# Kernel optimization log

Measured on AMD Instinct MI355X. Metric: run time of the kernel, lower is better.

Reference implementation:

```python
import jax, jax.numpy as jnp
import numpy as np
from jax import lax

B, T, V, E, H = 64, 20, 32000, 256, 512
EPS = 1e-5


def _conv_bn_relu(x, w, b, g, beta, m, v):
    # x: (B,C,H,W), w: (O,I,3,3), stride 2, pad 1; BN in eval mode with running stats
    y = lax.conv_general_dilated(x, w, (2, 2), ((1, 1), (1, 1)),
                                 dimension_numbers=('NCHW', 'OIHW', 'NCHW'))
    y = y + b[None, :, None, None]
    inv = g / jnp.sqrt(v + EPS)
    y = y * inv[None, :, None, None] + (beta - m * inv)[None, :, None, None]
    return jax.nn.relu(y)


def setup_inputs() -> dict:
    key = jax.random.key(0)
    ks = iter(jax.random.split(key, 40))
    s = 0.05
    d = {}
    d['images'] = jax.random.normal(next(ks), (B, 3, 64, 64), jnp.float32)
    d['captions'] = jax.random.randint(next(ks), (B, T), 0, V)
    chans = [3, 64, 128, 256, 512]
    for i in range(4):
        ci, co = chans[i], chans[i + 1]
        d[f'conv{i+1}_w'] = jax.random.normal(next(ks), (co, ci, 3, 3), jnp.float32) * s
        d[f'conv{i+1}_b'] = jnp.zeros((co,), jnp.float32)
        d[f'bn{i+1}_g'] = jnp.ones((co,), jnp.float32)
        d[f'bn{i+1}_b'] = jnp.zeros((co,), jnp.float32)
        d[f'bn{i+1}_m'] = jnp.zeros((co,), jnp.float32)
        d[f'bn{i+1}_v'] = jnp.ones((co,), jnp.float32)
    d['proj_w'] = jax.random.normal(next(ks), (E, 512), jnp.float32) * s
    d['proj_b'] = jnp.zeros((E,), jnp.float32)
    d['emb'] = jax.random.normal(next(ks), (V, E), jnp.float32) * s
    d['att_wv'] = jax.random.normal(next(ks), (H, E), jnp.float32) * s
    d['att_bv'] = jnp.zeros((H,), jnp.float32)
    d['att_wt'] = jax.random.normal(next(ks), (H, H), jnp.float32) * s
    d['att_bt'] = jnp.zeros((H,), jnp.float32)
    d['att_wa'] = jax.random.normal(next(ks), (1, H), jnp.float32) * s
    d['att_ba'] = jnp.zeros((1,), jnp.float32)
    d['w_ih'] = jax.random.normal(next(ks), (4 * H, 2 * E), jnp.float32) * s
    d['w_hh'] = jax.random.normal(next(ks), (4 * H, H), jnp.float32) * s
    d['b_ih'] = jnp.zeros((4 * H,), jnp.float32)
    d['b_hh'] = jnp.zeros((4 * H,), jnp.float32)
    d['out_w'] = jax.random.normal(next(ks), (V, H), jnp.float32) * s
    d['out_b'] = jnp.zeros((V,), jnp.float32)
    return d


def reference(images, captions,
              conv1_w, conv1_b, bn1_g, bn1_b, bn1_m, bn1_v,
              conv2_w, conv2_b, bn2_g, bn2_b, bn2_m, bn2_v,
              conv3_w, conv3_b, bn3_g, bn3_b, bn3_m, bn3_v,
              conv4_w, conv4_b, bn4_g, bn4_b, bn4_m, bn4_v,
              proj_w, proj_b, emb,
              att_wv, att_bv, att_wt, att_bt, att_wa, att_ba,
              w_ih, w_hh, b_ih, b_hh, out_w, out_b):
    # --- image encoder ---
    x = _conv_bn_relu(images, conv1_w, conv1_b, bn1_g, bn1_b, bn1_m, bn1_v)
    x = _conv_bn_relu(x, conv2_w, conv2_b, bn2_g, bn2_b, bn2_m, bn2_v)
    x = _conv_bn_relu(x, conv3_w, conv3_b, bn3_g, bn3_b, bn3_m, bn3_v)
    x = _conv_bn_relu(x, conv4_w, conv4_b, bn4_g, bn4_b, bn4_m, bn4_v)  # (B,512,4,4)
    b, c, h_, w_ = x.shape
    visual = x.reshape(b, c, h_ * w_).transpose(0, 2, 1)  # (B,R=16,512)
    visual = visual @ proj_w.T + proj_b                    # (B,R,E)

    v_proj = visual @ att_wv.T + att_bv                    # (B,R,H) - precompute

    emb_seq = emb[captions].transpose(1, 0, 2)             # (T,B,E)

    def step(carry, word_embed):
        h, cst = carry
        # attention over regions conditioned on previous h
        t = h @ att_wt.T + att_bt                          # (B,H)
        comb = jnp.tanh(v_proj + t[:, None, :])            # (B,R,H)
        scores = jnp.einsum('brh,h->br', comb, att_wa[0]) + att_ba[0]
        attw = jax.nn.softmax(scores, axis=1)              # (B,R)
        attended = jnp.einsum('br,bre->be', attw, visual)  # (B,E)
        xin = jnp.concatenate([word_embed, attended], axis=1)  # (B,2E)
        gates = xin @ w_ih.T + b_ih + h @ w_hh.T + b_hh    # (B,4H)
        i, f, g, o = jnp.split(gates, 4, axis=1)           # torch gate order i,f,g,o
        cst = jax.nn.sigmoid(f) * cst + jax.nn.sigmoid(i) * jnp.tanh(g)
        h = jax.nn.sigmoid(o) * jnp.tanh(cst)
        logits = h @ out_w.T + out_b                       # (B,V)
        return (h, cst), logits

    h0 = jnp.zeros((b, H), visual.dtype)
    c0 = jnp.zeros((b, H), visual.dtype)
    _, logits = lax.scan(step, (h0, c0), emb_seq)          # (T,B,V)
    return logits.transpose(1, 0, 2)                       # (B,T,V)
```

## Files before the change

kernel.cpp:

```cpp
#include <hip/hip_runtime.h>
#include <hip/hip_bf16.h>
#include <cstdint>
#include <cstddef>

typedef __attribute__((ext_vector_type(8))) short short8;
typedef __attribute__((ext_vector_type(4))) float floatx4;

__device__ inline float bf2f(unsigned short u) {
  union { unsigned int i; float f; } v; v.i = ((unsigned int)u) << 16; return v.f;
}
__device__ inline unsigned short f2bf(float f) {
  union { float f; unsigned int i; } v; v.f = f;
  unsigned int u = v.i;
  return (unsigned short)((u + 0x7FFFu + ((u >> 16) & 1u)) >> 16);
}
__device__ inline short8 ld8(const unsigned short* p) {
  return *reinterpret_cast<const short8*>(p);
}
__device__ inline float sigmoidf_(float x) { return 1.0f / (1.0f + expf(-x)); }

#define AT_LD(p)    __hip_atomic_load((p), __ATOMIC_RELAXED, __HIP_MEMORY_SCOPE_AGENT)
#define AT_ST(p, v) __hip_atomic_store((p), (v), __ATOMIC_RELAXED, __HIP_MEMORY_SCOPE_AGENT)
#define WAITCNT0()  asm volatile("s_waitcnt vmcnt(0) lgkmcnt(0)" ::: "memory")

static const size_t OFF_WIH   = 0;
static const size_t OFF_WHH   = 2097152;
static const size_t OFF_VPROJ = 4194304;
static const size_t OFF_VISE  = 5242880;
static const size_t OFF_HS    = 5767168;
static const size_t OFF_XIN   = 7077888;
static const size_t OFF_H0    = 7143424;
static const size_t OFF_H1    = 7208960;
static const size_t OFF_CT    = 7274496;
static const size_t OFF_W1PAD = 7405568;
static const size_t OFF_CW2   = 7409664;
static const size_t OFF_CW3   = 7557120;
static const size_t OFF_CW4   = 8146944;
static const size_t OFF_PRJW  = 10506240;
static const size_t OFF_ATWV  = 10768384;
static const size_t OFF_ACT1  = 11030528;
static const size_t OFF_ACT3  = 11030528;
static const size_t OFF_ACT2  = 19419136;
static const size_t OFF_ACT4  = 19419136;
static const size_t OFF_VISA  = 20467712;
static const size_t OFF_COL   = 23613440;
static const size_t OFF_BAR   = 28332032;
static const size_t OFF_ATWT  = 28348416;
static const size_t OFF_BIG   = 28872704;
static const size_t NEED_BIG  = OFF_BIG + 32768000;

__device__ inline void grid_bar(unsigned int* bar, unsigned int gen) {
  WAITCNT0();
  __syncthreads();
  if (threadIdx.x == 0)
    AT_ST(bar + (size_t)blockIdx.x * 32, gen);
  if (blockIdx.x == 0 && threadIdx.x < 64) {
    while (AT_LD(bar + (size_t)threadIdx.x * 32) < gen) __builtin_amdgcn_s_sleep(1);
    if (threadIdx.x == 0) AT_ST(bar + 2048, gen);
  }
  if (threadIdx.x == 0) {
    while (AT_LD(bar + 2048) < gen) __builtin_amdgcn_s_sleep(1);
  }
  __syncthreads();
  asm volatile("" ::: "memory");
}

__global__ void cvt_k(const float* __restrict__ s, unsigned short* __restrict__ d, int n4)
{
  int i = blockIdx.x * 256 + threadIdx.x;
  if (i < n4) {
    float4 v = reinterpret_cast<const float4*>(s)[i];
    ushort4 o;
    o.x = f2bf(v.x); o.y = f2bf(v.y); o.z = f2bf(v.z); o.w = f2bf(v.w);
    reinterpret_cast<ushort4*>(d)[i] = o;
  }
}

struct CvtArgs {
  const float* s[8];
  unsigned short* d[8];
  int cum[9];
};
__global__ void cvtall_k(CvtArgs a)
{
  int i = blockIdx.x * 256 + threadIdx.x;
  if (i >= a.cum[8]) return;
  int seg = 0;
  while (seg < 7 && i >= a.cum[seg + 1]) ++seg;
  int j = i - a.cum[seg];
  float4 v = reinterpret_cast<const float4*>(a.s[seg])[j];
  ushort4 o;
  o.x = f2bf(v.x); o.y = f2bf(v.y); o.z = f2bf(v.z); o.w = f2bf(v.w);
  reinterpret_cast<ushort4*>(a.d[seg])[j] = o;
}

__global__ void init_k(const float* __restrict__ conv1_w, unsigned short* __restrict__ w1pad,
                       unsigned short* __restrict__ h0, float* __restrict__ cT,
                       unsigned int* __restrict__ bar)
{
  int i = blockIdx.x * 256 + threadIdx.x;
  if (i < 64 * 32) {
    int co = i >> 5, k = i & 31;
    w1pad[i] = (k < 27) ? f2bf(conv1_w[co * 27 + k]) : (unsigned short)0;
  }
  if (i < 64 * 512) h0[i] = 0;
  if (i < 512 * 64) cT[i] = 0.0f;
  if (i < 4096) bar[i] = 0u;
}

__global__ void im2col1_k(const float* __restrict__ in, unsigned short* __restrict__ col)
{
  int o = blockIdx.x * 256 + threadIdx.x;
  int n = o >> 5, k = o & 31;
  unsigned short v = 0;
  if (k < 27) {
    int b = n >> 10, y = (n >> 5) & 31, x = n & 31;
    int ci = k / 9, r9 = k - ci * 9, ky = r9 / 3, kx = r9 - ky * 3;
    int iy = 2 * y - 1 + ky, ix = 2 * x - 1 + kx;
    if (iy >= 0 && iy < 64 && ix >= 0 && ix < 64)
      v = f2bf(in[(((size_t)b * 3 + ci) << 12) + (iy << 6) + ix]);
  }
  col[o] = v;
}

__global__ void im2col_k(const unsigned short* __restrict__ in, unsigned short* __restrict__ col,
                         int Cin, int Hin, int Win, int Kreal, int Kpad, int lgHW, int lgW,
                         int n0)
{
  const int ng = n0 + blockIdx.x;
  const int b = ng >> lgHW;
  const int yx = ng & ((1 << lgHW) - 1);
  const int y = yx >> lgW;
  const int x = yx & ((1 << lgW) - 1);
  const int iy0 = 2 * y - 1;
  const int ix0 = 2 * x - 1;
  for (int k = threadIdx.x; k < Kpad; k += blockDim.x) {
    unsigned short v = 0;
    if (k < Kreal) {
      int ci = k / 9;
      int r9 = k - ci * 9;
      int ky = r9 / 3;
      int kx = r9 - ky * 3;
      int iy = iy0 + ky, ix = ix0 + kx;
      if (iy >= 0 && iy < Hin && ix >= 0 && ix < Win) {
        size_t idx = (((size_t)b * Cin + ci) * Hin + iy) * Win + ix;
        v = in[idx];
      }
    }
    col[(size_t)blockIdx.x * Kpad + k] = v;
  }
}

__global__ void visa_k(const unsigned short* __restrict__ act4, unsigned short* __restrict__ visA)
{
  int o = blockIdx.x * 256 + threadIdx.x;
  int c = o & 511, br = o >> 9;
  int b = br >> 4, r = br & 15;
  visA[o] = act4[(((size_t)b * 512 + c) << 4) + r];
}

template<int EPI>
__global__ __launch_bounds__(256)
void gemm_k(const unsigned short* __restrict__ A, const unsigned short* __restrict__ B,
            int K, int N, void* __restrict__ outp,
            const float* __restrict__ cb, const float* __restrict__ bg,
            const float* __restrict__ bb, const float* __restrict__ bm,
            const float* __restrict__ bv, int Cout, int lgHW,
            const float* __restrict__ biasN, int n_base, int ldOut)
{
  const int w   = threadIdx.x >> 6;
  const int l   = threadIdx.x & 63;
  const int l15 = l & 15;
  const int q   = l >> 4;
  const int m0  = blockIdx.y * 64;
  const int n0  = blockIdx.x * 256 + w * 64;
  const unsigned short* Ap = A + (size_t)(m0 + l15) * K + q * 8;
  const unsigned short* Bp = B + (size_t)(n0 + l15) * K + q * 8;

  floatx4 acc[4][4];
  #pragma unroll
  for (int i = 0; i < 4; i++)
    #pragma unroll
    for (int j = 0; j < 4; j++)
      acc[i][j] = (floatx4){0.f, 0.f, 0.f, 0.f};

  for (int kc = 0; kc < K; kc += 32) {
    short8 a0 = ld8(Ap + kc);
    short8 a1 = ld8(Ap + (size_t)16 * K + kc);
    short8 a2 = ld8(Ap + (size_t)32 * K + kc);
    short8 a3 = ld8(Ap + (size_t)48 * K + kc);
    #pragma unroll
    for (int nf = 0; nf < 4; nf++) {
      short8 bf = ld8(Bp + (size_t)(nf * 16) * K + kc);
      acc[0][nf] = __builtin_amdgcn_mfma_f32_16x16x32_bf16(a0, bf, acc[0][nf], 0, 0, 0);
      acc[1][nf] = __builtin_amdgcn_mfma_f32_16x16x32_bf16(a1, bf, acc[1][nf], 0, 0, 0);
      acc[2][nf] = __builtin_amdgcn_mfma_f32_16x16x32_bf16(a2, bf, acc[2][nf], 0, 0, 0);
      acc[3][nf] = __builtin_amdgcn_mfma_f32_16x16x32_bf16(a3, bf, acc[3][nf], 0, 0, 0);
    }
  }
  #pragma unroll
  for (int mf = 0; mf < 4; mf++) {
    #pragma unroll
    for (int r = 0; r < 4; r++) {
      int m = m0 + mf * 16 + q * 4 + r;
      float scale = 1.0f, shift = 0.0f;
      if (EPI == 0) {
        float inv = bg[m] / sqrtf(bv[m] + 1e-5f);
        scale = inv;
        shift = (cb[m] - bm[m]) * inv + bb[m];
      }
      #pragma unroll
      for (int nf = 0; nf < 4; nf++) {
        int n = n0 + nf * 16 + l15;
        float c = acc[mf][nf][r];
        if (EPI == 0) {
          c = fmaxf(c * scale + shift, 0.0f);
          int ng = n_base + n;
          int bi = ng >> lgHW;
          int yx = ng & ((1 << lgHW) - 1);
          ((unsigned short*)outp)[(((size_t)bi * Cout + m) << lgHW) + yx] = f2bf(c);
        } else if (EPI == 1) {
          ((unsigned short*)outp)[(size_t)m * N + n] = f2bf(c + biasN[n]);
        } else {
          ((float*)outp)[(size_t)m * ldOut + n_base + n] = c + biasN[n_base + n];
        }
      }
    }
  }
}

__global__ __launch_bounds__(256)
void rec_k(const unsigned short* __restrict__ w_ih, const unsigned short* __restrict__ w_hh,
           const float* __restrict__ b_ih, const float* __restrict__ b_hh,
           const unsigned short* __restrict__ vproj, const unsigned short* __restrict__ visE,
           const unsigned short* __restrict__ atwt, const float* __restrict__ att_bt,
           const float* __restrict__ att_wa, const float* __restrict__ att_ba,
           const int* __restrict__ captions, const float* __restrict__ emb,
           unsigned int* xin_u, unsigned int* h0_u, unsigned int* h1_u,
           float* __restrict__ cT, unsigned short* __restrict__ hs,
           unsigned int* __restrict__ bar)
{
  __shared__ __align__(16) float sH[512];
  __shared__ float sT[512];
  __shared__ float sA[256];
  __shared__ float sSc[16];
  __shared__ float sAw[16];
  __shared__ __align__(16) unsigned short sB[16384];
  __shared__ float sG[4][16][64];

  const int tid = threadIdx.x;
  const int bid = blockIdx.x;
  const int w   = tid >> 6;
  const int l   = tid & 63;
  const int l15 = l & 15;
  const int q   = l >> 4;
  const int u0  = bid * 16;
  const int arow = w * 512 + u0 + l15;

  for (int t = 0; t < 20; ++t) {
    unsigned int* hin_u  = (t & 1) ? h1_u : h0_u;
    unsigned int* hout_u = (t & 1) ? h0_u : h1_u;

    {
      const int b = bid;
      unsigned int hv = AT_LD(hin_u + b * 256 + tid);
      sH[2 * tid]     = bf2f((unsigned short)(hv & 0xffffu));
      sH[2 * tid + 1] = bf2f((unsigned short)(hv >> 16));
      __syncthreads();

      {
        const unsigned short* w0 = atwt + (size_t)tid * 512;
        const unsigned short* w1 = w0 + (size_t)256 * 512;
        float a0 = 0.f, a1 = 0.f;
        #pragma unroll 2
        for (int k = 0; k < 512; k += 8) {
          short8 x0 = ld8(w0 + k);
          short8 x1 = ld8(w1 + k);
          #pragma unroll
          for (int j = 0; j < 8; ++j) {
            float hk = sH[k + j];
            a0 += bf2f((unsigned short)x0[j]) * hk;
            a1 += bf2f((unsigned short)x1[j]) * hk;
          }
        }
        sT[tid]       = a0 + att_bt[tid];
        sT[tid + 256] = a1 + att_bt[tid + 256];
      }
      __syncthreads();

      {
        int r = tid >> 4, l16 = tid & 15;
        const unsigned short* vp = vproj + ((size_t)b * 16 + r) * 512;
        float s = 0.0f;
        int k0 = l16 * 32;
        for (int k = k0; k < k0 + 32; k++)
          s += tanhf(bf2f(vp[k]) + sT[k]) * att_wa[k];
        for (int d = 8; d >= 1; d >>= 1) s += __shfl_down(s, d, 16);
        if (l16 == 0) sSc[r] = s + att_ba[0];
      }
      __syncthreads();

      if (tid < 16) {
        float s = sSc[tid];
        float m = s;
        for (int d = 8; d >= 1; d >>= 1) m = fmaxf(m, __shfl_xor(m, d, 16));
        float e = expf(s - m);
        float sum = e;
        for (int d = 8; d >= 1; d >>= 1) sum += __shfl_xor(sum, d, 16);
        sAw[tid] = e / sum;
      }
      __syncthreads();

      {
        float a = 0.0f;
        #pragma unroll
        for (int r = 0; r < 16; r++)
          a += sAw[r] * bf2f(visE[((size_t)b * 16 + r) * 256 + tid]);
        sA[tid] = a;
      }
      __syncthreads();

      if (tid < 128) {
        int cap = captions[b * 20 + t];
        float2 ev = *reinterpret_cast<const float2*>(emb + (size_t)cap * 256 + 2 * tid);
        AT_ST(xin_u + b * 256 + tid,
              (unsigned int)f2bf(ev.x) | ((unsigned int)f2bf(ev.y) << 16));
      } else {
        int j2 = 2 * (tid - 128);
        AT_ST(xin_u + b * 256 + tid,
              (unsigned int)f2bf(sA[j2]) | ((unsigned int)f2bf(sA[j2 + 1]) << 16));
      }
    }
    grid_bar(bar, 2 * t + 1);

    if (bid < 32) {
      floatx4 acc[4];
      #pragma unroll
      for (int nt = 0; nt < 4; nt++) acc[nt] = (floatx4){0.f, 0.f, 0.f, 0.f};

      #pragma unroll
      for (int src = 0; src < 2; ++src) {
        unsigned int* Bu = src ? hin_u : xin_u;
        const unsigned short* Arow = (src ? w_hh : w_ih) + (size_t)arow * 512;
        #pragma unroll
        for (int half = 0; half < 2; ++half) {
          __syncthreads();
          for (int i = tid; i < 8192; i += 256) {
            int row = i >> 7, cu = i & 127;
            unsigned int v = AT_LD(Bu + row * 256 + half * 128 + cu);
            reinterpret_cast<unsigned int*>(sB)[(row * 128 + cu) ^ ((row & 7) << 2)] = v;
          }
          __syncthreads();
          const unsigned short* Ap = Arow + half * 256 + q * 8;
          #pragma unroll
          for (int kc = 0; kc < 256; kc += 32) {
            short8 a = ld8(Ap + kc);
            #pragma unroll
            for (int nt = 0; nt < 4; ++nt) {
              int row = l15 + nt * 16;
              short8 bf = *reinterpret_cast<const short8*>(
                  sB + (((size_t)row * 256 + q * 8 + kc) ^ ((row & 7) << 3)));
              acc[nt] = __builtin_amdgcn_mfma_f32_16x16x32_bf16(a, bf, acc[nt], 0, 0, 0);
            }
          }
        }
      }
      #pragma unroll
      for (int nt = 0; nt < 4; nt++)
        #pragma unroll
        for (int r = 0; r < 4; r++)
          sG[w][q * 4 + r][nt * 16 + l15] = acc[nt][r];
      __syncthreads();

      const int batch = tid & 63;
      const int g0 = tid >> 6;
      #pragma unroll
      for (int s = 0; s < 4; s += 2) {
        float hn2[2];
        #pragma unroll
        for (int d = 0; d < 2; ++d) {
          int um = g0 * 4 + s + d;
          int u = u0 + um;
          float ii = sG[0][um][batch] + b_ih[u]        + b_hh[u];
          float ff = sG[1][um][batch] + b_ih[512 + u]  + b_hh[512 + u];
          float gg = sG[2][um][batch] + b_ih[1024 + u] + b_hh[1024 + u];
          float oo = sG[3][um][batch] + b_ih[1536 + u] + b_hh[1536 + u];
          float co = cT[u * 64 + batch];
          float cn = sigmoidf_(ff) * co + sigmoidf_(ii) * tanhf(gg);
          hn2[d] = sigmoidf_(oo) * tanhf(cn);
          cT[u * 64 + batch] = cn;
        }
        int u = u0 + g0 * 4 + s;
        unsigned int hp = (unsigned int)f2bf(hn2[0]) | ((unsigned int)f2bf(hn2[1]) << 16);
        AT_ST(hout_u + batch * 256 + (u >> 1), hp);
        *reinterpret_cast<unsigned int*>(hs + ((size_t)batch * 20 + t) * 512 + u) = hp;
      }
    }
    grid_bar(bar, 2 * t + 2);
  }
}

extern "C" void kernel_launch(void* const* d_in, const int* in_sizes, int n_in,
                              void* d_out, int out_size, void* d_ws, size_t ws_size,
                              hipStream_t stream)
{
  const float* images   = (const float*)d_in[0];
  const int*   captions = (const int*)d_in[1];
  const float* cw[4] = {(const float*)d_in[2],  (const float*)d_in[8],
                        (const float*)d_in[14], (const float*)d_in[20]};
  const float* cbp[4] = {(const float*)d_in[3],  (const float*)d_in[9],
                         (const float*)d_in[15], (const float*)d_in[21]};
  const float* bgp[4] = {(const float*)d_in[4],  (const float*)d_in[10],
                         (const float*)d_in[16], (const float*)d_in[22]};
  const float* bbp[4] = {(const float*)d_in[5],  (const float*)d_in[11],
                         (const float*)d_in[17], (const float*)d_in[23]};
  const float* bmp[4] = {(const float*)d_in[6],  (const float*)d_in[12],
                         (const float*)d_in[18], (const float*)d_in[24]};
  const float* bvp[4] = {(const float*)d_in[7],  (const float*)d_in[13],
                         (const float*)d_in[19], (const float*)d_in[25]};
  const float* proj_w = (const float*)d_in[26];
  const float* proj_b = (const float*)d_in[27];
  const float* emb    = (const float*)d_in[28];
  const float* att_wv = (const float*)d_in[29];
  const float* att_bv = (const float*)d_in[30];
  const float* att_wt = (const float*)d_in[31];
  const float* att_bt = (const float*)d_in[32];
  const float* att_wa = (const float*)d_in[33];
  const float* att_ba = (const float*)d_in[34];
  const float* w_ih   = (const float*)d_in[35];
  const float* w_hh   = (const float*)d_in[36];
  const float* b_ih   = (const float*)d_in[37];
  const float* b_hh   = (const float*)d_in[38];
  const float* out_w  = (const float*)d_in[39];
  const float* out_b  = (const float*)d_in[40];

  char* W = (char*)d_ws;
  unsigned short* wih_b = (unsigned short*)(W + OFF_WIH);
  unsigned short* whh_b = (unsigned short*)(W + OFF_WHH);
  unsigned short* vproj = (unsigned short*)(W + OFF_VPROJ);
  unsigned short* visE  = (unsigned short*)(W + OFF_VISE);
  unsigned short* hs    = (unsigned short*)(W + OFF_HS);
  unsigned short* xin   = (unsigned short*)(W + OFF_XIN);
  unsigned short* h0    = (unsigned short*)(W + OFF_H0);
  unsigned short* h1    = (unsigned short*)(W + OFF_H1);
  float*          cT    = (float*)(W + OFF_CT);
  unsigned short* w1pad = (unsigned short*)(W + OFF_W1PAD);
  unsigned short* cw2_b = (unsigned short*)(W + OFF_CW2);
  unsigned short* cw3_b = (unsigned short*)(W + OFF_CW3);
  unsigned short* cw4_b = (unsigned short*)(W + OFF_CW4);
  unsigned short* prw_b = (unsigned short*)(W + OFF_PRJW);
  unsigned short* awv_b = (unsigned short*)(W + OFF_ATWV);
  unsigned short* atwt_b= (unsigned short*)(W + OFF_ATWT);
  unsigned short* act1  = (unsigned short*)(W + OFF_ACT1);
  unsigned short* act2  = (unsigned short*)(W + OFF_ACT2);
  unsigned short* act3  = (unsigned short*)(W + OFF_ACT3);
  unsigned short* act4  = (unsigned short*)(W + OFF_ACT4);
  unsigned short* visA  = (unsigned short*)(W + OFF_VISA);
  unsigned short* col   = (unsigned short*)(W + OFF_COL);
  unsigned int*   bar   = (unsigned int*)(W + OFF_BAR);
  const bool big = (ws_size >= NEED_BIG);
  unsigned short* colb  = big ? (unsigned short*)(W + OFF_BIG) : col;

  init_k<<<128, 256, 0, stream>>>(cw[0], w1pad, h0, cT, bar);

  {
    CvtArgs ca;
    ca.s[0] = w_ih;   ca.d[0] = wih_b;
    ca.s[1] = w_hh;   ca.d[1] = whh_b;
    ca.s[2] = cw[1];  ca.d[2] = cw2_b;
    ca.s[3] = cw[2];  ca.d[3] = cw3_b;
    ca.s[4] = cw[3];  ca.d[4] = cw4_b;
    ca.s[5] = proj_w; ca.d[5] = prw_b;
    ca.s[6] = att_wv; ca.d[6] = awv_b;
    ca.s[7] = att_wt; ca.d[7] = atwt_b;
    int c0 = 0;
    int cnt[8] = {262144, 262144, 18432, 73728, 294912, 32768, 32768, 65536};
    ca.cum[0] = 0;
    for (int i = 0; i < 8; i++) { c0 += cnt[i]; ca.cum[i + 1] = c0; }
    cvtall_k<<<(c0 + 255) / 256, 256, 0, stream>>>(ca);
  }

  im2col1_k<<<8192, 256, 0, stream>>>(images, col);
  gemm_k<0><<<dim3(256, 1), 256, 0, stream>>>(w1pad, col, 32, 65536, act1,
      cbp[0], bgp[0], bbp[0], bmp[0], bvp[0], 64, 10, nullptr, 0, 0);

  if (big) {
    im2col_k<<<16384, 256, 0, stream>>>(act1, colb, 64, 32, 32, 576, 576, 8, 4, 0);
    gemm_k<0><<<dim3(64, 2), 256, 0, stream>>>(cw2_b, colb, 576, 16384, act2,
        cbp[1], bgp[1], bbp[1], bmp[1], bvp[1], 128, 8, nullptr, 0, 0);
    im2col_k<<<4096, 256, 0, stream>>>(act2, colb, 128, 16, 16, 1152, 1152, 6, 3, 0);
    gemm_k<0><<<dim3(16, 4), 256, 0, stream>>>(cw3_b, colb, 1152, 4096, act3,
        cbp[2], bgp[2], bbp[2], bmp[2], bvp[2], 256, 6, nullptr, 0, 0);
  } else {
    for (int c = 0; c < 4; c++) {
      im2col_k<<<4096, 256, 0, stream>>>(act1, col, 64, 32, 32, 576, 576, 8, 4, c * 4096);
      gemm_k<0><<<dim3(16, 2), 256, 0, stream>>>(cw2_b, col, 576, 4096, act2,
          cbp[1], bgp[1], bbp[1], bmp[1], bvp[1], 128, 8, nullptr, c * 4096, 0);
    }
    for (int c = 0; c < 2; c++) {
      im2col_k<<<2048, 256, 0, stream>>>(act2, col, 128, 16, 16, 1152, 1152, 6, 3, c * 2048);
      gemm_k<0><<<dim3(8, 4), 256, 0, stream>>>(cw3_b, col, 1152, 2048, act3,
          cbp[2], bgp[2], bbp[2], bmp[2], bvp[2], 256, 6, nullptr, c * 2048, 0);
    }
  }
  im2col_k<<<1024, 256, 0, stream>>>(act3, col, 256, 8, 8, 2304, 2304, 4, 2, 0);
  gemm_k<0><<<dim3(4, 8), 256, 0, stream>>>(cw4_b, col, 2304, 1024, act4,
      cbp[3], bgp[3], bbp[3], bmp[3], bvp[3], 512, 4, nullptr, 0, 0);

  visa_k<<<2048, 256, 0, stream>>>(act4, visA);
  gemm_k<1><<<dim3(1, 16), 256, 0, stream>>>(visA, prw_b, 512, 256, visE,
      nullptr, nullptr, nullptr, nullptr, nullptr, 0, 0, proj_b, 0, 0);
  gemm_k<1><<<dim3(2, 16), 256, 0, stream>>>(visE, awv_b, 256, 512, vproj,
      nullptr, nullptr, nullptr, nullptr, nullptr, 0, 0, att_bv, 0, 0);

  rec_k<<<64, 256, 0, stream>>>(wih_b, whh_b, b_ih, b_hh, vproj, visE,
                                atwt_b, att_bt, att_wa, att_ba, captions, emb,
                                (unsigned int*)xin, (unsigned int*)h0, (unsigned int*)h1,
                                cT, hs, bar);

  if (big) {
    unsigned short* owb = (unsigned short*)(W + OFF_BIG);
    cvt_k<<<16000, 256, 0, stream>>>(out_w, owb, 32000 * 512 / 4);
    gemm_k<2><<<dim3(125, 20), 256, 0, stream>>>(hs, owb, 512, 32000,
        d_out, nullptr, nullptr, nullptr, nullptr, nullptr, 0, 0, out_b, 0, 32000);
  } else {
    for (int c = 0; c < 8; c++) {
      int rows = (c < 7) ? 4096 : 3328;
      const float* src = out_w + (size_t)c * 4096 * 512;
      cvt_k<<<rows / 2, 256, 0, stream>>>(src, col, rows * 512 / 4);
      gemm_k<2><<<dim3(rows / 256, 20), 256, 0, stream>>>(hs, col, 512, rows,
          d_out, nullptr, nullptr, nullptr, nullptr, nullptr, 0, 0, out_b, c * 4096, 32000);
    }
  }
}
```

Baseline: 1.884 ms.

## Replace grid barriers with per-block flags and overlap LSTM gate GEMM segments

The recurrent kernel drops its two full grid barriers per timestep and uses per-block step flags instead. Gate blocks wait only on the h flags, then run the word-embedding and W_hh parts of the gate product while attention is still running, and wait on the attention flags only before the attended-vector segment. The cell state moves from global memory into registers, bias sums are precomputed once, and tanh, exp and sigmoid use fast __expf approximations. This cuts serialization and global traffic in the latency-bound recurrence, at the cost of slightly lower accuracy and a more delicate memory-ordering protocol.

After: 1.687 ms. 10.5% less time.

```diff
diff --git a/kernel.cpp b/kernel.cpp
--- a/kernel.cpp
+++ b/kernel.cpp
@@ -17,11 +17,16 @@
 __device__ inline short8 ld8(const unsigned short* p) {
   return *reinterpret_cast<const short8*>(p);
 }
-__device__ inline float sigmoidf_(float x) { return 1.0f / (1.0f + expf(-x)); }
+__device__ inline float sigmoidf_(float x) { return 1.0f / (1.0f + __expf(-x)); }
+__device__ inline float tanh_fast(float x) {
+  float e = __expf(2.0f * x);
+  return 1.0f - 2.0f / (e + 1.0f);
+}
 
 #define AT_LD(p)    __hip_atomic_load((p), __ATOMIC_RELAXED, __HIP_MEMORY_SCOPE_AGENT)
 #define AT_ST(p, v) __hip_atomic_store((p), (v), __ATOMIC_RELAXED, __HIP_MEMORY_SCOPE_AGENT)
 #define WAITCNT0()  asm volatile("s_waitcnt vmcnt(0) lgkmcnt(0)" ::: "memory")
+#define CFENCE()    asm volatile("" ::: "memory")
 
 static const size_t OFF_WIH   = 0;
 static const size_t OFF_WHH   = 2097152;
@@ -49,22 +54,6 @@
 static const size_t OFF_BIG   = 28872704;
 static const size_t NEED_BIG  = OFF_BIG + 32768000;
 
-__device__ inline void grid_bar(unsigned int* bar, unsigned int gen) {
-  WAITCNT0();
-  __syncthreads();
-  if (threadIdx.x == 0)
-    AT_ST(bar + (size_t)blockIdx.x * 32, gen);
-  if (blockIdx.x == 0 && threadIdx.x < 64) {
-    while (AT_LD(bar + (size_t)threadIdx.x * 32) < gen) __builtin_amdgcn_s_sleep(1);
-    if (threadIdx.x == 0) AT_ST(bar + 2048, gen);
-  }
-  if (threadIdx.x == 0) {
-    while (AT_LD(bar + 2048) < gen) __builtin_amdgcn_s_sleep(1);
-  }
-  __syncthreads();
-  asm volatile("" ::: "memory");
-}
-
 __global__ void cvt_k(const float* __restrict__ s, unsigned short* __restrict__ d, int n4)
 {
   int i = blockIdx.x * 256 + threadIdx.x;
@@ -95,8 +84,7 @@
 }
 
 __global__ void init_k(const float* __restrict__ conv1_w, unsigned short* __restrict__ w1pad,
-                       unsigned short* __restrict__ h0, float* __restrict__ cT,
-                       unsigned int* __restrict__ bar)
+                       unsigned short* __restrict__ h0, unsigned int* __restrict__ bar)
 {
   int i = blockIdx.x * 256 + threadIdx.x;
   if (i < 64 * 32) {
@@ -104,7 +92,6 @@
     w1pad[i] = (k < 27) ? f2bf(conv1_w[co * 27 + k]) : (unsigned short)0;
   }
   if (i < 64 * 512) h0[i] = 0;
-  if (i < 512 * 64) cT[i] = 0.0f;
   if (i < 4096) bar[i] = 0u;
 }
 
@@ -237,16 +224,18 @@
            const float* __restrict__ att_wa, const float* __restrict__ att_ba,
            const int* __restrict__ captions, const float* __restrict__ emb,
            unsigned int* xin_u, unsigned int* h0_u, unsigned int* h1_u,
-           float* __restrict__ cT, unsigned short* __restrict__ hs,
-           unsigned int* __restrict__ bar)
+           unsigned short* __restrict__ hs, unsigned int* __restrict__ bar)
 {
   __shared__ __align__(16) float sH[512];
   __shared__ float sT[512];
   __shared__ float sA[256];
   __shared__ float sSc[16];
   __shared__ float sAw[16];
-  __shared__ __align__(16) unsigned short sB[16384];
+  __shared__ __align__(16) unsigned short sB[64 * 256];
   __shared__ float sG[4][16][64];
+
+  unsigned int* xf = bar;
+  unsigned int* hf = bar + 64;
 
   const int tid = threadIdx.x;
   const int bid = blockIdx.x;
@@ -256,10 +245,63 @@
   const int q   = l >> 4;
   const int u0  = bid * 16;
   const int arow = w * 512 + u0 + l15;
+  const unsigned short* wihRow = w_ih + (size_t)arow * 512;
+  const unsigned short* whhRow = w_hh + (size_t)arow * 512;
+
+  float creg[4];
+  float bsum[4][4];
+  if (bid < 32) {
+    const int batch = tid & 63;
+    const int g0 = tid >> 6;
+    (void)batch;
+    #pragma unroll
+    for (int s = 0; s < 4; ++s) {
+      creg[s] = 0.0f;
+      int u = u0 + g0 * 4 + s;
+      #pragma unroll
+      for (int g = 0; g < 4; ++g)
+        bsum[s][g] = b_ih[g * 512 + u] + b_hh[g * 512 + u];
+    }
+  }
+
+  #define STAGE_TILE(SRC_EXPR)                                              \
+    {                                                                       \
+      _Pragma("unroll")                                                     \
+      for (int i_ = 0; i_ < 16; ++i_) {                                     \
+        int p_ = i_ * 256 + tid;                                            \
+        int row_ = p_ >> 6, cu_ = p_ & 63;                                  \
+        unsigned long long v_ = (SRC_EXPR);                                 \
+        reinterpret_cast<unsigned long long*>(sB)[(row_ * 64 + cu_) ^ ((row_ & 7) << 1)] = v_; \
+      }                                                                     \
+    }
+
+  #define MFMA_SEG(APTR)                                                    \
+    {                                                                       \
+      const unsigned short* Ap_ = (APTR);                                   \
+      _Pragma("unroll")                                                     \
+      for (int kc = 0; kc < 256; kc += 32) {                                \
+        short8 a_ = ld8(Ap_ + kc);                                          \
+        _Pragma("unroll")                                                   \
+        for (int nt = 0; nt < 4; ++nt) {                                    \
+          int row_ = l15 + nt * 16;                                         \
+          short8 bf_ = *reinterpret_cast<const short8*>(                    \
+              sB + ((row_ * 256 + q * 8 + kc) ^ ((row_ & 7) << 3)));        \
+          acc[nt] = __builtin_amdgcn_mfma_f32_16x16x32_bf16(a_, bf_, acc[nt], 0, 0, 0); \
+        }                                                                   \
+      }                                                                     \
+    }
 
   for (int t = 0; t < 20; ++t) {
     unsigned int* hin_u  = (t & 1) ? h1_u : h0_u;
     unsigned int* hout_u = (t & 1) ? h0_u : h1_u;
+
+    if (t > 0) {
+      if (tid < 32) {
+        while ((int)AT_LD(hf + tid) < t) __builtin_amdgcn_s_sleep(1);
+      }
+      __syncthreads();
+      CFENCE();
+    }
 
     {
       const int b = bid;
@@ -292,9 +334,11 @@
         int r = tid >> 4, l16 = tid & 15;
         const unsigned short* vp = vproj + ((size_t)b * 16 + r) * 512;
         float s = 0.0f;
-        int k0 = l16 * 32;
-        for (int k = k0; k < k0 + 32; k++)
-          s += tanhf(bf2f(vp[k]) + sT[k]) * att_wa[k];
+        #pragma unroll 4
+        for (int i = 0; i < 32; ++i) {
+          int k = i * 16 + l16;
+          s += tanh_fast(bf2f(vp[k]) + sT[k]) * att_wa[k];
+        }
         for (int d = 8; d >= 1; d >>= 1) s += __shfl_down(s, d, 16);
         if (l16 == 0) sSc[r] = s + att_ba[0];
       }
@@ -304,7 +348,7 @@
         float s = sSc[tid];
         float m = s;
         for (int d = 8; d >= 1; d >>= 1) m = fmaxf(m, __shfl_xor(m, d, 16));
-        float e = expf(s - m);
+        float e = __expf(s - m);
         float sum = e;
         for (int d = 8; d >= 1; d >>= 1) sum += __shfl_xor(sum, d, 16);
         sAw[tid] = e / sum;
@@ -321,50 +365,60 @@
       __syncthreads();
 
       if (tid < 128) {
-        int cap = captions[b * 20 + t];
-        float2 ev = *reinterpret_cast<const float2*>(emb + (size_t)cap * 256 + 2 * tid);
-        AT_ST(xin_u + b * 256 + tid,
-              (unsigned int)f2bf(ev.x) | ((unsigned int)f2bf(ev.y) << 16));
-      } else {
-        int j2 = 2 * (tid - 128);
-        AT_ST(xin_u + b * 256 + tid,
-              (unsigned int)f2bf(sA[j2]) | ((unsigned int)f2bf(sA[j2 + 1]) << 16));
-      }
-    }
-    grid_bar(bar, 2 * t + 1);
+        AT_ST(xin_u + b * 128 + tid,
+              (unsigned int)f2bf(sA[2 * tid]) | ((unsigned int)f2bf(sA[2 * tid + 1]) << 16));
+      }
+      WAITCNT0();
+      __syncthreads();
+      if (tid == 0) AT_ST(xf + bid, (unsigned int)(t + 1));
+    }
 
     if (bid < 32) {
       floatx4 acc[4];
       #pragma unroll
       for (int nt = 0; nt < 4; nt++) acc[nt] = (floatx4){0.f, 0.f, 0.f, 0.f};
 
-      #pragma unroll
-      for (int src = 0; src < 2; ++src) {
-        unsigned int* Bu = src ? hin_u : xin_u;
-        const unsigned short* Arow = (src ? w_hh : w_ih) + (size_t)arow * 512;
+      {
         #pragma unroll
-        for (int half = 0; half < 2; ++half) {
-          __syncthreads();
-          for (int i = tid; i < 8192; i += 256) {
-            int row = i >> 7, cu = i & 127;
-            unsigned int v = AT_LD(Bu + row * 256 + half * 128 + cu);
-            reinterpret_cast<unsigned int*>(sB)[(row * 128 + cu) ^ ((row & 7) << 2)] = v;
-          }
-          __syncthreads();
-          const unsigned short* Ap = Arow + half * 256 + q * 8;
-          #pragma unroll
-          for (int kc = 0; kc < 256; kc += 32) {
-            short8 a = ld8(Ap + kc);
-            #pragma unroll
-            for (int nt = 0; nt < 4; ++nt) {
-              int row = l15 + nt * 16;
-              short8 bf = *reinterpret_cast<const short8*>(
-                  sB + (((size_t)row * 256 + q * 8 + kc) ^ ((row & 7) << 3)));
-              acc[nt] = __builtin_amdgcn_mfma_f32_16x16x32_bf16(a, bf, acc[nt], 0, 0, 0);
-            }
-          }
+        for (int i_ = 0; i_ < 16; ++i_) {
+          int p_ = i_ * 256 + tid;
+          int row_ = p_ >> 6, c4_ = p_ & 63;
+          int cap_ = captions[row_ * 20 + t];
+          float4 ev = *reinterpret_cast<const float4*>(emb + (size_t)cap_ * 256 + c4_ * 4);
+          unsigned long long v_ =
+              (unsigned long long)f2bf(ev.x) |
+              ((unsigned long long)f2bf(ev.y) << 16) |
+              ((unsigned long long)f2bf(ev.z) << 32) |
+              ((unsigned long long)f2bf(ev.w) << 48);
+          reinterpret_cast<unsigned long long*>(sB)[(row_ * 64 + c4_) ^ ((row_ & 7) << 1)] = v_;
         }
       }
+      __syncthreads();
+      MFMA_SEG(wihRow + q * 8);
+      __syncthreads();
+
+      const unsigned long long* hull = reinterpret_cast<const unsigned long long*>(hin_u);
+      STAGE_TILE(AT_LD(hull + ((i_ * 256 + tid) >> 6) * 128 + ((i_ * 256 + tid) & 63)));
+      __syncthreads();
+      MFMA_SEG(whhRow + q * 8);
+      __syncthreads();
+      STAGE_TILE(AT_LD(hull + ((i_ * 256 + tid) >> 6) * 128 + 64 + ((i_ * 256 + tid) & 63)));
+      __syncthreads();
+      MFMA_SEG(whhRow + 256 + q * 8);
+      __syncthreads();
+
+      if (tid < 64) {
+        while ((int)AT_LD(xf + tid) < t + 1) __builtin_amdgcn_s_sleep(1);
+      }
+      __syncthreads();
+      CFENCE();
+
+      const unsigned long long* xull = reinterpret_cast<const unsigned long long*>(xin_u);
+      STAGE_TILE(AT_LD(xull + ((i_ * 256 + tid) >> 6) * 64 + ((i_ * 256 + tid) & 63)));
+      __syncthreads();
+      MFMA_SEG(wihRow + 256 + q * 8);
+      __syncthreads();
+
       #pragma unroll
       for (int nt = 0; nt < 4; nt++)
         #pragma unroll
@@ -380,24 +434,26 @@
         #pragma unroll
         for (int d = 0; d < 2; ++d) {
           int um = g0 * 4 + s + d;
-          int u = u0 + um;
-          float ii = sG[0][um][batch] + b_ih[u]        + b_hh[u];
-          float ff = sG[1][um][batch] + b_ih[512 + u]  + b_hh[512 + u];
-          float gg = sG[2][um][batch] + b_ih[1024 + u] + b_hh[1024 + u];
-          float oo = sG[3][um][batch] + b_ih[1536 + u] + b_hh[1536 + u];
-          float co = cT[u * 64 + batch];
-          float cn = sigmoidf_(ff) * co + sigmoidf_(ii) * tanhf(gg);
-          hn2[d] = sigmoidf_(oo) * tanhf(cn);
-          cT[u * 64 + batch] = cn;
+          float ii = sG[0][um][batch] + bsum[s + d][0];
+          float ff = sG[1][um][batch] + bsum[s + d][1];
+          float gg = sG[2][um][batch] + bsum[s + d][2];
+          float oo = sG[3][um][batch] + bsum[s + d][3];
+          float cn = sigmoidf_(ff) * creg[s + d] + sigmoidf_(ii) * tanh_fast(gg);
+          hn2[d] = sigmoidf_(oo) * tanh_fast(cn);
+          creg[s + d] = cn;
         }
         int u = u0 + g0 * 4 + s;
         unsigned int hp = (unsigned int)f2bf(hn2[0]) | ((unsigned int)f2bf(hn2[1]) << 16);
         AT_ST(hout_u + batch * 256 + (u >> 1), hp);
         *reinterpret_cast<unsigned int*>(hs + ((size_t)batch * 20 + t) * 512 + u) = hp;
       }
-    }
-    grid_bar(bar, 2 * t + 2);
-  }
+      WAITCNT0();
+      __syncthreads();
+      if (tid == 0) AT_ST(hf + bid, (unsigned int)(t + 1));
+    }
+  }
+  #undef STAGE_TILE
+  #undef MFMA_SEG
 }
 
 extern "C" void kernel_launch(void* const* d_in, const int* in_sizes, int n_in,
@@ -443,7 +499,6 @@
   unsigned short* xin   = (unsigned short*)(W + OFF_XIN);
   unsigned short* h0    = (unsigned short*)(W + OFF_H0);
   unsigned short* h1    = (unsigned short*)(W + OFF_H1);
-  float*          cT    = (float*)(W + OFF_CT);
   unsigned short* w1pad = (unsigned short*)(W + OFF_W1PAD);
   unsigned short* cw2_b = (unsigned short*)(W + OFF_CW2);
   unsigned short* cw3_b = (unsigned short*)(W + OFF_CW3);
@@ -461,7 +516,7 @@
   const bool big = (ws_size >= NEED_BIG);
   unsigned short* colb  = big ? (unsigned short*)(W + OFF_BIG) : col;
 
-  init_k<<<128, 256, 0, stream>>>(cw[0], w1pad, h0, cT, bar);
+  init_k<<<128, 256, 0, stream>>>(cw[0], w1pad, h0, bar);
 
   {
     CvtArgs ca;
@@ -516,7 +571,7 @@
   rec_k<<<64, 256, 0, stream>>>(wih_b, whh_b, b_ih, b_hh, vproj, visE,
                                 atwt_b, att_bt, att_wa, att_ba, captions, emb,
                                 (unsigned int*)xin, (unsigned int*)h0, (unsigned int*)h1,
-                                cT, hs, bar);
+                                hs, bar);
 
   if (big) {
     unsigned short* owb = (unsigned short*)(W + OFF_BIG);
```
